# Kernel tuning notes

Hardware: AMD Instinct MI355X
Metric: run time of the kernel (lower is better)

Reference implementation:

```python
import jax, jax.numpy as jnp
import numpy as np

SIZE = 256

def _linear(x, W, b):
    # torch nn.Linear: y = x @ W^T + b, W has shape [out, in]
    return jnp.einsum('bsd,ed->bse', x, W) + b

def setup_inputs() -> dict:
    key = jax.random.key(0)
    ks = jax.random.split(key, 10)
    B, Sq, Sk, D = 8, 2048, 2048, SIZE
    s = 1.0 / np.sqrt(D)
    return {
        'x': jax.random.normal(ks[0], (B, Sq, D), jnp.float32),
        'states': jax.random.normal(ks[1], (B, Sk, D), jnp.float32),
        'Wq': jax.random.normal(ks[2], (D, D), jnp.float32) * s,
        'bq': jnp.zeros((D,), jnp.float32),
        'Wk': jax.random.normal(ks[3], (D, D), jnp.float32) * s,
        'bk': jnp.zeros((D,), jnp.float32),
        'Wv': jax.random.normal(ks[4], (D, D), jnp.float32) * s,
        'bv': jnp.zeros((D,), jnp.float32),
        'Wa': jax.random.normal(ks[5], (D, D), jnp.float32) * s,  # LuongAttention.fc
        'ba': jnp.zeros((D,), jnp.float32),
    }

def reference(x, states, Wq, bq, Wk, bk, Wv, bv, Wa, ba):
    q = _linear(x, Wq, bq)          # [B,Sq,D]
    k = _linear(states, Wk, bk)     # [B,Sk,D]
    v = _linear(states, Wv, bv)     # [B,Sk,D]
    wk = _linear(k, Wa, ba)         # [B,Sk,D]
    scores = jnp.einsum('bqd,bkd->bqk', q, wk)   # bmm(q, wk^T)
    scores = jax.nn.softmax(scores, axis=-1)
    # original: (v[:,None,:,:] * scores[...,None]).sum(-2) == matmul
    context = jnp.einsum('bqk,bkd->bqd', scores, v)
    return context
```

## Files before the change

kernel.cpp:

```cpp
#include <hip/hip_runtime.h>
#include <cstdint>
#include <cstddef>

typedef _Float16 half_t;
typedef _Float16 half8 __attribute__((ext_vector_type(8)));
typedef _Float16 half4v __attribute__((ext_vector_type(4)));
typedef float float4_ __attribute__((ext_vector_type(4)));

#define NB 8
#define SEQ 2048
#define DIM 256
#define NROWS (NB*SEQ)
#define KS 4
#define NIT 16

__device__ __forceinline__ void dma16(const half_t* g, half_t* l) {
    __builtin_amdgcn_global_load_lds(
        (const __attribute__((address_space(1))) void*)g,
        (__attribute__((address_space(3))) void*)l,
        16, 0, 0);
}

__global__ __launch_bounds__(256) void prep_kernel(
    const float* __restrict__ Wq, const float* __restrict__ Wk,
    const float* __restrict__ Wv, const float* __restrict__ Wa,
    const float* __restrict__ bq,
    half_t* __restrict__ M_hi, half_t* __restrict__ M_lo,
    half_t* __restrict__ Wk_hi, half_t* __restrict__ Wk_lo,
    half_t* __restrict__ Wv_hi, float* __restrict__ bq2)
{
    __shared__ float sWa[256];
    __shared__ float sred[256];
    const int d = blockIdx.x;
    const int m = threadIdx.x;
    sWa[m] = Wa[m * 256 + d];
    __syncthreads();

    float a0 = 0.f, a1 = 0.f, a2 = 0.f, a3 = 0.f;
    #pragma unroll 8
    for (int e = 0; e < 256; e += 4) {
        a0 += sWa[e + 0] * Wq[(e + 0) * 256 + m];
        a1 += sWa[e + 1] * Wq[(e + 1) * 256 + m];
        a2 += sWa[e + 2] * Wq[(e + 2) * 256 + m];
        a3 += sWa[e + 3] * Wq[(e + 3) * 256 + m];
    }
    float acc = (a0 + a1) + (a2 + a3);

    const int pos  = (((m >> 3) ^ (d & 7)) << 3) | (m & 7);
    const int sidx = d * 256 + pos;
    const int idx  = d * 256 + m;

    half_t h = (half_t)acc;
    M_hi[sidx] = h;
    M_lo[sidx] = (half_t)(acc - (float)h);
    float wk = Wk[idx];
    h = (half_t)wk;
    Wk_hi[sidx] = h;
    Wk_lo[sidx] = (half_t)(wk - (float)h);
    Wv_hi[sidx] = (half_t)Wv[idx];

    sred[m] = bq[m] * sWa[m];
    __syncthreads();
    #pragma unroll
    for (int s = 128; s > 0; s >>= 1) {
        if (m < s) sred[m] += sred[m + s];
        __syncthreads();
    }
    if (m == 0) bq2[d] = sred[0];
}

__global__ __launch_bounds__(256, 2) void linear_kernel(
    const float* __restrict__ x, const float* __restrict__ states,
    const half_t* __restrict__ M_hi, const half_t* __restrict__ M_lo, const float* __restrict__ bq2,
    const half_t* __restrict__ Wk_hi, const half_t* __restrict__ Wk_lo, const float* __restrict__ bk,
    const half_t* __restrict__ Wv_hi, const float* __restrict__ bv,
    half_t* __restrict__ q2_hi,
    half_t* __restrict__ k_hi,
    half_t* __restrict__ vT)
{
    __shared__ half_t sB[2 * 64 * 256];
    half_t* sBh = sB;
    half_t* sBl = sB + 64 * 256;

    const int seg  = blockIdx.x >> 8;
    const int t    = blockIdx.x & 255;
    const int tid  = threadIdx.x;
    const int lane = tid & 63;
    const int wv   = tid >> 6;
    const int quad = lane >> 4;
    const int l15  = lane & 15;
    const int rb   = t * 64;
    const int r0   = rb + wv * 16;

    const float* src  = (seg == 0) ? x : states;
    const half_t* Bh  = (seg == 0) ? M_hi : (seg == 1) ? Wk_hi : Wv_hi;
    const half_t* Bl  = (seg == 0) ? M_lo : Wk_lo;
    const float* bias = (seg == 0) ? bq2 : (seg == 1) ? bk : bv;

    half8 ah[8], al[8];
    #pragma unroll
    for (int c = 0; c < 8; ++c) {
        const float* pa = src + (size_t)(r0 + l15) * 256 + c * 32 + quad * 8;
        float4_ u0 = *(const float4_*)pa;
        float4_ u1 = *(const float4_*)(pa + 4);
        #pragma unroll
        for (int j = 0; j < 4; ++j) {
            half_t hh = (half_t)u0[j];
            ah[c][j] = hh; al[c][j] = (half_t)(u0[j] - (float)hh);
            hh = (half_t)u1[j];
            ah[c][4 + j] = hh; al[c][4 + j] = (half_t)(u1[j] - (float)hh);
        }
    }

    float4_ acc[16];
    if (seg != 2) {
        #pragma unroll
        for (int nt = 0; nt < 16; ++nt) {
            float be = bias[nt * 16 + l15];
            acc[nt] = {be, be, be, be};
        }
    } else {
        #pragma unroll
        for (int et = 0; et < 16; ++et)
            #pragma unroll
            for (int r = 0; r < 4; ++r)
                acc[et][r] = bias[et * 16 + quad * 4 + r];
    }

    #pragma unroll
    for (int eg = 0; eg < 4; ++eg) {
        __syncthreads();
        {
            const half_t* src_h = Bh + (size_t)eg * 16384;
            #pragma unroll
            for (int i = 0; i < 8; ++i) {
                const int sg = i * 4 + wv;
                dma16(src_h + sg * 512 + lane * 8, sBh + sg * 512);
            }
            if (seg != 2) {
                const half_t* src_l = Bl + (size_t)eg * 16384;
                #pragma unroll
                for (int i = 0; i < 8; ++i) {
                    const int sg = i * 4 + wv;
                    dma16(src_l + sg * 512 + lane * 8, sBl + sg * 512);
                }
            }
        }
        __syncthreads();

        if (seg != 2) {
            #pragma unroll
            for (int ntl = 0; ntl < 4; ++ntl) {
                float4_ a = acc[eg * 4 + ntl];
                const int el = ntl * 16 + l15;
                #pragma unroll
                for (int c = 0; c < 8; ++c) {
                    int off = el * 256 + (((c * 4 + quad) ^ (el & 7)) * 8);
                    half8 bh = *(const half8*)(sBh + off);
                    half8 bl = *(const half8*)(sBl + off);
                    a = __builtin_amdgcn_mfma_f32_16x16x32_f16(ah[c], bh, a, 0, 0, 0);
                    a = __builtin_amdgcn_mfma_f32_16x16x32_f16(al[c], bh, a, 0, 0, 0);
                    a = __builtin_amdgcn_mfma_f32_16x16x32_f16(ah[c], bl, a, 0, 0, 0);
                }
                acc[eg * 4 + ntl] = a;
            }
        } else {
            #pragma unroll
            for (int ntl = 0; ntl < 4; ++ntl) {
                float4_ a = acc[eg * 4 + ntl];
                const int el = ntl * 16 + l15;
                #pragma unroll
                for (int c = 0; c < 8; ++c) {
                    int off = el * 256 + (((c * 4 + quad) ^ (el & 7)) * 8);
                    half8 aw = *(const half8*)(sBh + off);
                    a = __builtin_amdgcn_mfma_f32_16x16x32_f16(aw, ah[c], a, 0, 0, 0);
                }
                acc[eg * 4 + ntl] = a;
            }
        }
    }

    __syncthreads();
    if (seg != 2) {
        half_t* R = sB;
        #pragma unroll
        for (int nt = 0; nt < 16; ++nt)
            #pragma unroll
            for (int r = 0; r < 4; ++r)
                R[(wv * 16 + quad * 4 + r) * 256 + nt * 16 + l15] = (half_t)acc[nt][r];
        __syncthreads();
        if (seg == 0) {
            for (int i = 0; i < 8; ++i) {
                int g = tid + i * 256;
                int row = g >> 5, cc = g & 31;
                *(half8*)(q2_hi + (size_t)(rb + row) * 256 + cc * 8) =
                    *(const half8*)(R + row * 256 + cc * 8);
            }
        } else {
            for (int i = 0; i < 8; ++i) {
                int g = tid + i * 256;
                int row = g >> 5, cc = g & 31;
                int s = row & 31;
                size_t dst = ((size_t)(rb + row) >> 5) * 8192 + s * 256 + ((cc ^ (s & 7)) * 8);
                *(half8*)(k_hi + dst) = *(const half8*)(R + row * 256 + cc * 8);
            }
        }
    } else {
        half_t* sV = sB;
        #pragma unroll
        for (int et = 0; et < 16; ++et)
            #pragma unroll
            for (int r = 0; r < 4; ++r)
                sV[(et * 16 + quad * 4 + r) * 68 + wv * 16 + l15] = (half_t)acc[et][r];
        __syncthreads();
        const int b = rb >> 11, s0 = rb & 2047;
        for (int i = 0; i < 8; ++i) {
            int g = tid + i * 256;
            int d = g >> 3, sc8 = g & 7;
            int kt = (s0 >> 5) + (sc8 >> 2);
            int q  = sc8 & 3;
            int t32 = (sc8 >> 2) * 32;
            int slot = q ^ (d & 3) ^ ((d >> 2) & 3);
            half4v a4 = *(const half4v*)(sV + d * 68 + t32 + q * 4);
            half4v b4 = *(const half4v*)(sV + d * 68 + t32 + 16 + q * 4);
            half8 hv;
            hv[0] = a4[0]; hv[1] = a4[1]; hv[2] = a4[2]; hv[3] = a4[3];
            hv[4] = b4[0]; hv[5] = b4[1]; hv[6] = b4[2]; hv[7] = b4[3];
            size_t dst = ((size_t)b * 64 + kt) * 8192 + d * 32 + slot * 8;
            *(half8*)(vT + dst) = hv;
        }
    }
}

__global__ __launch_bounds__(256, 2) void attn_kernel(
    const half_t* __restrict__ q2_hi,
    const half_t* __restrict__ k_hi, const half_t* __restrict__ vT,
    half_t* __restrict__ pc, float* __restrict__ pm, float* __restrict__ pl)
{
    __shared__ __align__(16) unsigned char smem[64 * 1024];
    float* scr = (float*)smem;

    const int tid  = threadIdx.x;
    const int lane = tid & 63;
    const int wv   = tid >> 6;
    const int quad = lane >> 4;
    const int l15  = lane & 15;

    const int b  = blockIdx.x & 7;
    const int qt = (blockIdx.x >> 3) & 15;
    const int ks = blockIdx.x >> 7;

    const int qbase = b * 2048 + qt * 128 + wv * 32;

    half8 qf[2][8];
    #pragma unroll
    for (int ct = 0; ct < 2; ++ct)
        #pragma unroll
        for (int c = 0; c < 8; ++c)
            qf[ct][c] = *(const half8*)(q2_hi +
                (size_t)(qbase + ct * 16 + l15) * 256 + c * 32 + quad * 8);

    float4_ ctx[16][2];
    #pragma unroll
    for (int dt = 0; dt < 16; ++dt) {
        ctx[dt][0] = {0.f, 0.f, 0.f, 0.f};
        ctx[dt][1] = {0.f, 0.f, 0.f, 0.f};
    }
    float m_c[2] = {-1e30f, -1e30f};
    float l_c[2] = {0.f, 0.f};

    const half_t* kh_b = k_hi + (size_t)b * 64 * 8192;
    const half_t* vt_b = vT   + (size_t)b * 64 * 8192;
    const int t0 = ks * NIT;

    const int vslot8 = (quad ^ (l15 & 3) ^ ((l15 >> 2) & 3)) * 8;

    {
        const half_t* kt_ = kh_b + (size_t)t0 * 8192;
        #pragma unroll
        for (int i = 0; i < 4; ++i) {
            const int sg = i * 4 + wv;
            dma16(kt_ + sg * 512 + lane * 8, (half_t*)smem + sg * 512);
        }
        const half_t* vt_ = vt_b + (size_t)t0 * 8192;
        #pragma unroll
        for (int i = 0; i < 4; ++i) {
            const int sg = i * 4 + wv;
            dma16(vt_ + sg * 512 + lane * 8, (half_t*)(smem + 32768) + sg * 512);
        }
    }

    half8 pfp[2];
    #pragma unroll
    for (int ct = 0; ct < 2; ++ct)
        #pragma unroll
        for (int j = 0; j < 8; ++j) pfp[ct][j] = (half_t)0;

    for (int it = 0; it < NIT; ++it) {
        half_t* s_k  = (half_t*)(smem + ((it & 1) << 14));
        half_t* s_vP = (half_t*)(smem + 32768 + (((it + 1) & 1) << 14));
        const bool pre = (it + 1 < NIT);

        asm volatile("s_waitcnt vmcnt(4)" ::: "memory");
        __builtin_amdgcn_s_barrier();
        asm volatile("" ::: "memory");

        if (pre) {
            const half_t* kt_ = kh_b + (size_t)(t0 + it + 1) * 8192;
            half_t* kdst = (half_t*)(smem + (((it + 1) & 1) << 14));
            #pragma unroll
            for (int i = 0; i < 4; ++i) {
                const int sg = i * 4 + wv;
                dma16(kt_ + sg * 512 + lane * 8, kdst + sg * 512);
            }
        }

        float4_ S[2][2];
        S[0][0] = {0.f,0.f,0.f,0.f}; S[0][1] = {0.f,0.f,0.f,0.f};
        S[1][0] = {0.f,0.f,0.f,0.f}; S[1][1] = {0.f,0.f,0.f,0.f};
        __builtin_amdgcn_s_setprio(1);
        #pragma unroll
        for (int c = 0; c < 8; ++c) {
            #pragma unroll
            for (int kt = 0; kt < 2; ++kt) {
                const int key = kt * 16 + l15;
                const int off = key * 256 + (((c * 4 + quad) ^ (key & 7)) * 8);
                half8 kf = *(const half8*)(s_k + off);
                #pragma unroll
                for (int ct = 0; ct < 2; ++ct)
                    S[kt][ct] = __builtin_amdgcn_mfma_f32_16x16x32_f16(kf, qf[ct][c], S[kt][ct], 0, 0, 0);
            }
            if (it > 0) {
                #pragma unroll
                for (int dl = 0; dl < 2; ++dl) {
                    const int dt = c * 2 + dl;
                    half8 vf = *(const half8*)(s_vP + (dt * 16 + l15) * 32 + vslot8);
                    ctx[dt][0] = __builtin_amdgcn_mfma_f32_16x16x32_f16(vf, pfp[0], ctx[dt][0], 0, 0, 0);
                    ctx[dt][1] = __builtin_amdgcn_mfma_f32_16x16x32_f16(vf, pfp[1], ctx[dt][1], 0, 0, 0);
                }
            }
        }
        __builtin_amdgcn_s_setprio(0);
        __builtin_amdgcn_sched_barrier(0);
        __builtin_amdgcn_s_barrier();
        asm volatile("" ::: "memory");

        if (pre) {
            const half_t* vt_ = vt_b + (size_t)(t0 + it + 1) * 8192;
            half_t* vdst = (half_t*)(smem + 32768 + (((it + 1) & 1) << 14));
            #pragma unroll
            for (int i = 0; i < 4; ++i) {
                const int sg = i * 4 + wv;
                dma16(vt_ + sg * 512 + lane * 8, vdst + sg * 512);
            }
        }

        float mx0, mx1;
        {
            float a0 = fmaxf(fmaxf(S[0][0][0], S[0][0][1]), fmaxf(S[0][0][2], S[0][0][3]));
            float b0 = fmaxf(fmaxf(S[1][0][0], S[1][0][1]), fmaxf(S[1][0][2], S[1][0][3]));
            mx0 = fmaxf(a0, b0);
            float a1 = fmaxf(fmaxf(S[0][1][0], S[0][1][1]), fmaxf(S[0][1][2], S[0][1][3]));
            float b1 = fmaxf(fmaxf(S[1][1][0], S[1][1][1]), fmaxf(S[1][1][2], S[1][1][3]));
            mx1 = fmaxf(a1, b1);
        }
        const int doresc = __any((mx0 > m_c[0] + 8.f) || (mx1 > m_c[1] + 8.f));
        float alpha0 = 1.f, alpha1 = 1.f;
        if (doresc) {
            float r0 = fmaxf(mx0, __shfl_xor(mx0, 16));
            r0 = fmaxf(r0, __shfl_xor(r0, 32));
            float r1 = fmaxf(mx1, __shfl_xor(mx1, 16));
            r1 = fmaxf(r1, __shfl_xor(r1, 32));
            float mn0 = fmaxf(m_c[0], r0);
            float mn1 = fmaxf(m_c[1], r1);
            alpha0 = __expf(m_c[0] - mn0);
            alpha1 = __expf(m_c[1] - mn1);
            m_c[0] = mn0; m_c[1] = mn1;
        }
        half8 pfc[2];
        #pragma unroll
        for (int ct = 0; ct < 2; ++ct) {
            const float mm = m_c[ct];
            float rs = 0.f;
            #pragma unroll
            for (int r = 0; r < 4; ++r) {
                float p0 = __expf(S[0][ct][r] - mm);
                float p1 = __expf(S[1][ct][r] - mm);
                rs += p0 + p1;
                pfc[ct][r]     = (half_t)p0;
                pfc[ct][4 + r] = (half_t)p1;
            }
            l_c[ct] = l_c[ct] * (ct ? alpha1 : alpha0) + rs;
        }
        if (doresc) {
            #pragma unroll
            for (int dt = 0; dt < 16; ++dt)
                #pragma unroll
                for (int r = 0; r < 4; ++r) {
                    ctx[dt][0][r] *= alpha0;
                    ctx[dt][1][r] *= alpha1;
                }
        }
        pfp[0] = pfc[0];
        pfp[1] = pfc[1];
    }

    asm volatile("s_waitcnt vmcnt(0)" ::: "memory");
    __builtin_amdgcn_s_barrier();
    asm volatile("" ::: "memory");
    {
        half_t* s_v = (half_t*)(smem + 32768 + (((NIT - 1) & 1) << 14));
        __builtin_amdgcn_s_setprio(1);
        #pragma unroll
        for (int dt = 0; dt < 16; ++dt) {
            half8 vf = *(const half8*)(s_v + (dt * 16 + l15) * 32 + vslot8);
            ctx[dt][0] = __builtin_amdgcn_mfma_f32_16x16x32_f16(vf, pfp[0], ctx[dt][0], 0, 0, 0);
            ctx[dt][1] = __builtin_amdgcn_mfma_f32_16x16x32_f16(vf, pfp[1], ctx[dt][1], 0, 0, 0);
        }
        __builtin_amdgcn_s_setprio(0);
    }

    float lt[2];
    #pragma unroll
    for (int ct = 0; ct < 2; ++ct) {
        float s = l_c[ct];
        s += __shfl_xor(s, 16);
        s += __shfl_xor(s, 32);
        lt[ct] = s;
    }

    float rinv[2] = {1.0f / lt[0], 1.0f / lt[1]};
    float* sw = scr + wv * (32 * 68);
    half_t* pcs = pc + (size_t)ks * NROWS * 256;
    #pragma unroll
    for (int rd = 0; rd < 4; ++rd) {
        #pragma unroll
        for (int dtl = 0; dtl < 4; ++dtl) {
            const int dt = rd * 4 + dtl;
            #pragma unroll
            for (int ct = 0; ct < 2; ++ct)
                #pragma unroll
                for (int r = 0; r < 4; ++r)
                    sw[(ct * 16 + l15) * 68 + dtl * 16 + quad * 4 + r] = ctx[dt][ct][r] * rinv[ct];
        }
        #pragma unroll
        for (int i = 0; i < 8; ++i) {
            int g = lane + i * 64;
            int q = g >> 4, dc = g & 15;
            float4_ v4 = *(const float4_*)(sw + q * 68 + dc * 4);
            half4v h4;
            #pragma unroll
            for (int j = 0; j < 4; ++j) h4[j] = (half_t)v4[j];
            *(half4v*)(pcs + (size_t)(qbase + q) * 256 + rd * 64 + dc * 4) = h4;
        }
    }
    if (quad == 0) {
        #pragma unroll
        for (int ct = 0; ct < 2; ++ct) {
            const size_t row = qbase + ct * 16 + l15;
            pm[(size_t)ks * NROWS + row] = m_c[ct];
            pl[(size_t)ks * NROWS + row] = lt[ct];
        }
    }
}

__global__ __launch_bounds__(256) void combine_kernel(
    const half_t* __restrict__ pc, const float* __restrict__ pm,
    const float* __restrict__ pl, float* __restrict__ out)
{
    const int t = threadIdx.x;
    const int row = blockIdx.x * 4 + (t >> 6);
    const int d0 = (t & 63) * 4;
    float m[KS], l[KS];
    float ms = -1e30f;
    #pragma unroll
    for (int i = 0; i < KS; ++i) {
        m[i] = pm[(size_t)i * NROWS + row];
        l[i] = pl[(size_t)i * NROWS + row];
        ms = fmaxf(ms, m[i]);
    }
    float w[KS], tot = 0.f;
    #pragma unroll
    for (int i = 0; i < KS; ++i) {
        w[i] = l[i] * __expf(m[i] - ms);
        tot += w[i];
    }
    float inv = 1.0f / tot;
    float4_ o = {0.f, 0.f, 0.f, 0.f};
    #pragma unroll
    for (int i = 0; i < KS; ++i) {
        half4v y = *(const half4v*)(pc + ((size_t)i * NROWS + row) * 256 + d0);
        float wi = w[i] * inv;
        #pragma unroll
        for (int j = 0; j < 4; ++j) o[j] += wi * (float)y[j];
    }
    *(float4_*)(out + (size_t)row * 256 + d0) = o;
}

extern "C" void kernel_launch(void* const* d_in, const int* in_sizes, int n_in,
                              void* d_out, int out_size, void* d_ws, size_t ws_size,
                              hipStream_t stream) {
    const float* x      = (const float*)d_in[0];
    const float* states = (const float*)d_in[1];
    const float* Wq     = (const float*)d_in[2];
    const float* bq     = (const float*)d_in[3];
    const float* Wk     = (const float*)d_in[4];
    const float* bk     = (const float*)d_in[5];
    const float* Wv     = (const float*)d_in[6];
    const float* bv     = (const float*)d_in[7];
    const float* Wa     = (const float*)d_in[8];
    float* out = (float*)d_out;

    char* ws = (char*)d_ws;
    size_t off = 0;
    auto alloc = [&](size_t bytes) -> void* {
        void* p = ws + off;
        off += (bytes + 255) & ~(size_t)255;
        return p;
    };
    half_t* M_hi  = (half_t*)alloc(65536 * 2);
    half_t* M_lo  = (half_t*)alloc(65536 * 2);
    half_t* Wk_hi = (half_t*)alloc(65536 * 2);
    half_t* Wk_lo = (half_t*)alloc(65536 * 2);
    half_t* Wv_hi = (half_t*)alloc(65536 * 2);
    float*  bq2   = (float*)alloc(256 * 4);
    half_t* q2_hi = (half_t*)alloc((size_t)NROWS * 256 * 2);
    half_t* k_hi  = (half_t*)alloc((size_t)NROWS * 256 * 2);
    half_t* vT    = (half_t*)alloc((size_t)NROWS * 256 * 2);
    half_t* pc    = (half_t*)alloc((size_t)KS * NROWS * 256 * 2);
    float*  pm    = (float*)alloc((size_t)KS * NROWS * 4);
    float*  pl    = (float*)alloc((size_t)KS * NROWS * 4);

    prep_kernel<<<256, 256, 0, stream>>>(Wq, Wk, Wv, Wa, bq,
                                         M_hi, M_lo, Wk_hi, Wk_lo, Wv_hi, bq2);
    linear_kernel<<<768, 256, 0, stream>>>(x, states,
                                           M_hi, M_lo, bq2,
                                           Wk_hi, Wk_lo, bk,
                                           Wv_hi, bv,
                                           q2_hi, k_hi, vT);
    attn_kernel<<<8 * 16 * KS, 256, 0, stream>>>(q2_hi, k_hi, vT,
                                                 pc, pm, pl);
    combine_kernel<<<NROWS / 4, 256, 0, stream>>>(pc, pm, pl, out);
}
```

Before: 179.2 us.

## Double-buffer weight staging in linear kernel to overlap DMA with MFMA

The weight tile loop in linear_kernel goes from four 64-row stages to eight 32-row half-stages held in two LDS buffers. The next half-stage is prefetched with global_load_lds while the current one feeds the MFMAs, and each iteration needs only one barrier. This aims to hide the global-to-LDS latency that previously stalled every stage between two __syncthreads. The risks are the extra loop iterations and barriers, plus possible scratch use if the compiler does not fully unroll the runtime-indexed accumulator array.

```diff
diff --git a/kernel.cpp b/kernel.cpp
--- a/kernel.cpp
+++ b/kernel.cpp
@@ -79,8 +79,6 @@
     half_t* __restrict__ vT)
 {
     __shared__ half_t sB[2 * 64 * 256];
-    half_t* sBh = sB;
-    half_t* sBl = sB + 64 * 256;
 
     const int seg  = blockIdx.x >> 8;
     const int t    = blockIdx.x & 255;
@@ -97,6 +95,8 @@
     const half_t* Bl  = (seg == 0) ? M_lo : Wk_lo;
     const float* bias = (seg == 0) ? bq2 : (seg == 1) ? bk : bv;
 
+    const int hgsz = (seg != 2) ? 16384 : 8192;
+
     half8 ah[8], al[8];
     #pragma unroll
     for (int c = 0; c < 8; ++c) {
@@ -127,57 +127,62 @@
                 acc[et][r] = bias[et * 16 + quad * 4 + r];
     }
 
-    #pragma unroll
-    for (int eg = 0; eg < 4; ++eg) {
-        __syncthreads();
-        {
-            const half_t* src_h = Bh + (size_t)eg * 16384;
-            #pragma unroll
-            for (int i = 0; i < 8; ++i) {
+    auto stage = [&](int h, half_t* dst) {
+        const half_t* src_h = Bh + (size_t)h * 8192;
+        #pragma unroll
+        for (int i = 0; i < 4; ++i) {
+            const int sg = i * 4 + wv;
+            dma16(src_h + sg * 512 + lane * 8, dst + sg * 512);
+        }
+        if (seg != 2) {
+            const half_t* src_l = Bl + (size_t)h * 8192;
+            #pragma unroll
+            for (int i = 0; i < 4; ++i) {
                 const int sg = i * 4 + wv;
-                dma16(src_h + sg * 512 + lane * 8, sBh + sg * 512);
-            }
-            if (seg != 2) {
-                const half_t* src_l = Bl + (size_t)eg * 16384;
-                #pragma unroll
-                for (int i = 0; i < 8; ++i) {
-                    const int sg = i * 4 + wv;
-                    dma16(src_l + sg * 512 + lane * 8, sBl + sg * 512);
-                }
-            }
-        }
-        __syncthreads();
-
+                dma16(src_l + sg * 512 + lane * 8, dst + 8192 + sg * 512);
+            }
+        }
+    };
+
+    stage(0, sB);
+    for (int h = 0; h < 8; ++h) {
+        asm volatile("s_waitcnt vmcnt(0)" ::: "memory");
+        __builtin_amdgcn_s_barrier();
+        asm volatile("" ::: "memory");
+        if (h < 7) stage(h + 1, sB + ((h + 1) & 1) * hgsz);
+
+        half_t* bufh = sB + (h & 1) * hgsz;
         if (seg != 2) {
             #pragma unroll
-            for (int ntl = 0; ntl < 4; ++ntl) {
-                float4_ a = acc[eg * 4 + ntl];
+            for (int ntl = 0; ntl < 2; ++ntl) {
+                float4_ a = acc[h * 2 + ntl];
                 const int el = ntl * 16 + l15;
                 #pragma unroll
                 for (int c = 0; c < 8; ++c) {
                     int off = el * 256 + (((c * 4 + quad) ^ (el & 7)) * 8);
-                    half8 bh = *(const half8*)(sBh + off);
-                    half8 bl = *(const half8*)(sBl + off);
+                    half8 bh = *(const half8*)(bufh + off);
+                    half8 bl = *(const half8*)(bufh + 8192 + off);
                     a = __builtin_amdgcn_mfma_f32_16x16x32_f16(ah[c], bh, a, 0, 0, 0);
                     a = __builtin_amdgcn_mfma_f32_16x16x32_f16(al[c], bh, a, 0, 0, 0);
                     a = __builtin_amdgcn_mfma_f32_16x16x32_f16(ah[c], bl, a, 0, 0, 0);
                 }
-                acc[eg * 4 + ntl] = a;
+                acc[h * 2 + ntl] = a;
             }
         } else {
             #pragma unroll
-            for (int ntl = 0; ntl < 4; ++ntl) {
-                float4_ a = acc[eg * 4 + ntl];
+            for (int ntl = 0; ntl < 2; ++ntl) {
+                float4_ a = acc[h * 2 + ntl];
                 const int el = ntl * 16 + l15;
                 #pragma unroll
                 for (int c = 0; c < 8; ++c) {
                     int off = el * 256 + (((c * 4 + quad) ^ (el & 7)) * 8);
-                    half8 aw = *(const half8*)(sBh + off);
+                    half8 aw = *(const half8*)(bufh + off);
                     a = __builtin_amdgcn_mfma_f32_16x16x32_f16(aw, ah[c], a, 0, 0, 0);
                 }
-                acc[eg * 4 + ntl] = a;
-            }
-        }
+                acc[h * 2 + ntl] = a;
+            }
+        }
+        __builtin_amdgcn_sched_barrier(0);
     }
 
     __syncthreads();
```

Result: no change. 177.0 us (-1.3%).
